# Performance work log

Hardware: AMD Instinct MI355X
Metric: run time of the kernel (lower is better)

The kernel has to match this reference:

```python
import jax, jax.numpy as jnp
import numpy as np

# Static SMPL kinematic tree (24 joints)
PARENTS = [-1, 0, 0, 0, 1, 2, 3, 4, 5, 6, 7, 8, 9, 9, 9, 12, 13, 14, 16, 17, 18, 19, 20, 21]
NJ = 24      # num joints
FS = 6       # local_feature_size
NF = 7       # bone_dim (1) + FS


def _topo_order(parents):
    children = {i: [] for i in range(len(parents))}
    roots = []
    for i, p in enumerate(parents):
        (roots if p == -1 else children[p]).append(i)
    order = []
    queue = roots[:]
    while queue:
        c = queue.pop(0)
        order.append(c)
        queue.extend(sorted(children[c]))
    return order

TOPO = _topo_order(PARENTS)


def setup_inputs() -> dict:
    key = jax.random.key(0)
    ks = jax.random.split(key, 5)
    B = 524288
    x = jax.random.normal(ks[0], (B, NJ, 1), dtype=jnp.float32)
    s = 1.0 / np.sqrt(NF)
    # Stacked per-joint weights. For the root joint, the parent-feature rows of
    # W1 are multiplied by a zero virtual parent feature, which is exactly
    # equivalent to the original Linear(1, 7) root MLP.
    W1 = jax.random.uniform(ks[1], (NJ, NF, NF), jnp.float32, -s, s)
    b1 = jax.random.uniform(ks[2], (NJ, NF), jnp.float32, -s, s)
    W2 = jax.random.uniform(ks[3], (NJ, NF, FS), jnp.float32, -s, s)
    b2 = jax.random.uniform(ks[4], (NJ, FS), jnp.float32, -s, s)
    return {"x": x, "W1": W1, "b1": b1, "W2": W2, "b2": b2}


def reference(x, W1, b1, W2, b2):
    # x: [B, NJ, 1]; sequential propagation over the fixed kinematic tree.
    B = x.shape[0]
    feats = [None] * NJ
    zero_pf = jnp.zeros((B, FS), x.dtype)
    for i in TOPO:
        p = PARENTS[i]
        pf = zero_pf if p == -1 else feats[p]
        inp = jnp.concatenate([x[:, i, :], pf], axis=-1)  # [B, 7]
        h = jax.nn.relu(inp @ W1[i] + b1[i])               # [B, 7]
        feats[i] = jax.nn.relu(h @ W2[i] + b2[i])          # [B, 6]
    return jnp.concatenate(feats, axis=-1)                 # [B, 144]
```

## Files before the change

### kernel.cpp

```cpp
#include <hip/hip_runtime.h>

#define NJ 24
#define NF 7
#define FS 6
#define THREADS 256
#define CUNITS 12
#define PAD 13

typedef float v4f __attribute__((ext_vector_type(4)));

__device__ constexpr int kParents[NJ] = {-1, 0, 0, 0, 1, 2, 3, 4, 5, 6, 7, 8,
                                          9, 9, 9, 12, 13, 14, 16, 17, 18, 19, 20, 21};

__global__ __launch_bounds__(THREADS, 3) void se1d_kernel(
    const float* __restrict__ x,
    const float* __restrict__ W1,
    const float* __restrict__ b1,
    const float* __restrict__ W2,
    const float* __restrict__ b2,
    float* __restrict__ out, int B)
{
    __shared__ float4 sm[THREADS / 64][64 * PAD];

    const int t    = threadIdx.x;
    const int lane = t & 63;
    const int wid  = t >> 6;
    const int b    = blockIdx.x * THREADS + t;
    const int wb   = blockIdx.x * THREADS + wid * 64;

    float4* const myStage = &sm[wid][lane * PAD];
    v4f* const outv = reinterpret_cast<v4f*>(out);

    float xr[NJ];
    {
        const v4f* xv = reinterpret_cast<const v4f*>(x + (size_t)b * NJ);
        #pragma unroll
        for (int c = 0; c < NJ / 4; ++c) {
            v4f v = __builtin_nontemporal_load(xv + c);
            xr[c * 4 + 0] = v.x; xr[c * 4 + 1] = v.y;
            xr[c * 4 + 2] = v.z; xr[c * 4 + 3] = v.w;
        }
    }

    float feats[NJ][FS];

    #pragma unroll
    for (int i = 0; i < NJ; ++i) {
        const int p = kParents[i];

        float inp[NF];
        inp[0] = xr[i];
        #pragma unroll
        for (int j = 0; j < FS; ++j) inp[1 + j] = (p < 0) ? 0.0f : feats[p][j];

        float h[NF];
        #pragma unroll
        for (int j = 0; j < NF; ++j) h[j] = b1[i * NF + j];
        #pragma unroll
        for (int k = 0; k < NF; ++k) {
            const float a = inp[k];
            #pragma unroll
            for (int j = 0; j < NF; ++j)
                h[j] = fmaf(a, W1[i * NF * NF + k * NF + j], h[j]);
        }
        #pragma unroll
        for (int j = 0; j < NF; ++j) h[j] = fmaxf(h[j], 0.0f);

        float f[FS];
        #pragma unroll
        for (int j = 0; j < FS; ++j) f[j] = b2[i * FS + j];
        #pragma unroll
        for (int k = 0; k < NF; ++k) {
            const float a = h[k];
            #pragma unroll
            for (int j = 0; j < FS; ++j)
                f[j] = fmaf(a, W2[i * NF * FS + k * FS + j], f[j]);
        }
        #pragma unroll
        for (int j = 0; j < FS; ++j) {
            f[j] = fmaxf(f[j], 0.0f);
            feats[i][j] = f[j];
        }

        if (i & 1) {
            const int pp = (i >> 1) & 3;
            float4* st = myStage + pp * 3;
            st[0] = make_float4(feats[i - 1][0], feats[i - 1][1],
                                feats[i - 1][2], feats[i - 1][3]);
            st[1] = make_float4(feats[i - 1][4], feats[i - 1][5], f[0], f[1]);
            st[2] = make_float4(f[2], f[3], f[4], f[5]);
        }

        if ((i & 7) == 7) {
            const int c = i >> 3;
            #pragma unroll
            for (int j = 0; j < CUNITS; ++j) {
                const int G = j * 64 + lane;
                const int s = G / CUNITS;
                const int q = G - s * CUNITS;
                float4 v = sm[wid][s * PAD + q];
                __builtin_nontemporal_store(
                    *reinterpret_cast<v4f*>(&v),
                    outv + (size_t)wb * 36 + c * 12 + s * 36 + q);
            }
        }
    }
    (void)B;
}

extern "C" void kernel_launch(void* const* d_in, const int* in_sizes, int n_in,
                              void* d_out, int out_size, void* d_ws, size_t ws_size,
                              hipStream_t stream) {
    const float* x  = (const float*)d_in[0];
    const float* W1 = (const float*)d_in[1];
    const float* b1 = (const float*)d_in[2];
    const float* W2 = (const float*)d_in[3];
    const float* b2 = (const float*)d_in[4];
    float* out = (float*)d_out;
    const int B = in_sizes[0] / NJ;
    const int grid = B / THREADS;
    hipLaunchKernelGGL(se1d_kernel, dim3(grid), dim3(THREADS), 0, stream,
                       x, W1, b1, W2, b2, out, B);
}
```

Measured before the change: 96.30 us.

## Split each block into a compute wavefront and a store wavefront via shared staging

Each 128-thread block now handles 64 batch rows. Wavefront 0 computes all 24 joints and stages every feature in shared memory, then after a barrier wavefront 1 writes the whole 36-float4-per-row output tile with coalesced stores. The intent is to take the output-store work off the compute wavefront and let the store wave of one block overlap with the compute of other blocks. In exchange, half of each block's threads sit idle during compute, shared memory per block grows to about 37 KB, and the nontemporal load and store hints are dropped.

```diff
diff --git a/kernel.cpp b/kernel.cpp
--- a/kernel.cpp
+++ b/kernel.cpp
@@ -3,16 +3,14 @@
 #define NJ 24
 #define NF 7
 #define FS 6
-#define THREADS 256
-#define CUNITS 12
-#define PAD 13
+#define SROW 37
 
 typedef float v4f __attribute__((ext_vector_type(4)));
 
 __device__ constexpr int kParents[NJ] = {-1, 0, 0, 0, 1, 2, 3, 4, 5, 6, 7, 8,
                                           9, 9, 9, 12, 13, 14, 16, 17, 18, 19, 20, 21};
 
-__global__ __launch_bounds__(THREADS, 3) void se1d_kernel(
+__global__ __launch_bounds__(128, 2) void se1d_kernel(
     const float* __restrict__ x,
     const float* __restrict__ W1,
     const float* __restrict__ b1,
@@ -20,89 +18,91 @@
     const float* __restrict__ b2,
     float* __restrict__ out, int B)
 {
-    __shared__ float4 sm[THREADS / 64][64 * PAD];
+    __shared__ v4f sm[64 * SROW];
 
     const int t    = threadIdx.x;
     const int lane = t & 63;
     const int wid  = t >> 6;
-    const int b    = blockIdx.x * THREADS + t;
-    const int wb   = blockIdx.x * THREADS + wid * 64;
+    const int base = blockIdx.x * 64;
 
-    float4* const myStage = &sm[wid][lane * PAD];
-    v4f* const outv = reinterpret_cast<v4f*>(out);
+    if (wid == 0) {
+        const int b = base + lane;
 
-    float xr[NJ];
-    {
-        const v4f* xv = reinterpret_cast<const v4f*>(x + (size_t)b * NJ);
+        float xr[NJ];
+        {
+            const v4f* xv = reinterpret_cast<const v4f*>(x + (size_t)b * NJ);
+            #pragma unroll
+            for (int c = 0; c < NJ / 4; ++c) {
+                v4f v = xv[c];
+                xr[c * 4 + 0] = v.x; xr[c * 4 + 1] = v.y;
+                xr[c * 4 + 2] = v.z; xr[c * 4 + 3] = v.w;
+            }
+        }
+
+        float feats[NJ][FS];
+        v4f* const myStage = &sm[lane * SROW];
+
         #pragma unroll
-        for (int c = 0; c < NJ / 4; ++c) {
-            v4f v = __builtin_nontemporal_load(xv + c);
-            xr[c * 4 + 0] = v.x; xr[c * 4 + 1] = v.y;
-            xr[c * 4 + 2] = v.z; xr[c * 4 + 3] = v.w;
+        for (int i = 0; i < NJ; ++i) {
+            const int p = kParents[i];
+
+            float inp[NF];
+            inp[0] = xr[i];
+            #pragma unroll
+            for (int j = 0; j < FS; ++j)
+                inp[1 + j] = (p < 0) ? 0.0f : feats[p][j];
+
+            float h[NF];
+            #pragma unroll
+            for (int j = 0; j < NF; ++j) h[j] = b1[i * NF + j];
+            #pragma unroll
+            for (int k = 0; k < NF; ++k) {
+                const float a = inp[k];
+                #pragma unroll
+                for (int j = 0; j < NF; ++j)
+                    h[j] = fmaf(a, W1[i * NF * NF + k * NF + j], h[j]);
+            }
+            #pragma unroll
+            for (int j = 0; j < NF; ++j) h[j] = fmaxf(h[j], 0.0f);
+
+            float f[FS];
+            #pragma unroll
+            for (int j = 0; j < FS; ++j) f[j] = b2[i * FS + j];
+            #pragma unroll
+            for (int k = 0; k < NF; ++k) {
+                const float a = h[k];
+                #pragma unroll
+                for (int j = 0; j < FS; ++j)
+                    f[j] = fmaf(a, W2[i * NF * FS + k * FS + j], f[j]);
+            }
+            #pragma unroll
+            for (int j = 0; j < FS; ++j) {
+                f[j] = fmaxf(f[j], 0.0f);
+                feats[i][j] = f[j];
+            }
+
+            if (i & 1) {
+                const int pp = i >> 1;
+                v4f* st = myStage + pp * 3;
+                st[0] = (v4f){feats[i - 1][0], feats[i - 1][1],
+                              feats[i - 1][2], feats[i - 1][3]};
+                st[1] = (v4f){feats[i - 1][4], feats[i - 1][5], f[0], f[1]};
+                st[2] = (v4f){f[2], f[3], f[4], f[5]};
+            }
         }
     }
 
-    float feats[NJ][FS];
+    __syncthreads();
 
-    #pragma unroll
-    for (int i = 0; i < NJ; ++i) {
-        const int p = kParents[i];
-
-        float inp[NF];
-        inp[0] = xr[i];
+    if (wid == 1) {
+        v4f* const outv = reinterpret_cast<v4f*>(out) + (size_t)base * 36;
         #pragma unroll
-        for (int j = 0; j < FS; ++j) inp[1 + j] = (p < 0) ? 0.0f : feats[p][j];
-
-        float h[NF];
-        #pragma unroll
-        for (int j = 0; j < NF; ++j) h[j] = b1[i * NF + j];
-        #pragma unroll
-        for (int k = 0; k < NF; ++k) {
-            const float a = inp[k];
-            #pragma unroll
-            for (int j = 0; j < NF; ++j)
-                h[j] = fmaf(a, W1[i * NF * NF + k * NF + j], h[j]);
-        }
-        #pragma unroll
-        for (int j = 0; j < NF; ++j) h[j] = fmaxf(h[j], 0.0f);
-
-        float f[FS];
-        #pragma unroll
-        for (int j = 0; j < FS; ++j) f[j] = b2[i * FS + j];
-        #pragma unroll
-        for (int k = 0; k < NF; ++k) {
-            const float a = h[k];
-            #pragma unroll
-            for (int j = 0; j < FS; ++j)
-                f[j] = fmaf(a, W2[i * NF * FS + k * FS + j], f[j]);
-        }
-        #pragma unroll
-        for (int j = 0; j < FS; ++j) {
-            f[j] = fmaxf(f[j], 0.0f);
-            feats[i][j] = f[j];
-        }
-
-        if (i & 1) {
-            const int pp = (i >> 1) & 3;
-            float4* st = myStage + pp * 3;
-            st[0] = make_float4(feats[i - 1][0], feats[i - 1][1],
-                                feats[i - 1][2], feats[i - 1][3]);
-            st[1] = make_float4(feats[i - 1][4], feats[i - 1][5], f[0], f[1]);
-            st[2] = make_float4(f[2], f[3], f[4], f[5]);
-        }
-
-        if ((i & 7) == 7) {
-            const int c = i >> 3;
-            #pragma unroll
-            for (int j = 0; j < CUNITS; ++j) {
-                const int G = j * 64 + lane;
-                const int s = G / CUNITS;
-                const int q = G - s * CUNITS;
-                float4 v = sm[wid][s * PAD + q];
-                __builtin_nontemporal_store(
-                    *reinterpret_cast<v4f*>(&v),
-                    outv + (size_t)wb * 36 + c * 12 + s * 36 + q);
-            }
+        for (int j = 0; j < 36; ++j) {
+            const int G = j * 64 + lane;
+            const int s = G / 36;
+            const int q = G - s * 36;
+            v4f v = sm[s * SROW + q];
+            outv[G] = v;
         }
     }
     (void)B;
@@ -118,7 +118,7 @@
     const float* b2 = (const float*)d_in[4];
     float* out = (float*)d_out;
     const int B = in_sizes[0] / NJ;
-    const int grid = B / THREADS;
-    hipLaunchKernelGGL(se1d_kernel, dim3(grid), dim3(THREADS), 0, stream,
+    const int grid = B / 64;
+    hipLaunchKernelGGL(se1d_kernel, dim3(grid), dim3(128), 0, stream,
                        x, W1, b1, W2, b2, out, B);
 }
```

New measurement: 128.1 us. 33.0% more time.
